# Kernel tuning notes

Measured on AMD Instinct MI355X. Metric: run time of the kernel, lower is better.

The kernel has to match this reference:

```python
import jax, jax.numpy as jnp
import numpy as np

B, T, I, H = 64, 2048, 256, 256  # batch, timesteps, input_dim, units


def setup_inputs() -> dict:
    key = jax.random.key(0)
    k1, k2, k3 = jax.random.split(key, 3)
    scale_x = 1.0 / np.sqrt(I)
    scale_h = 1.0 / np.sqrt(H)
    return {
        "x": jax.random.normal(k1, (B, T, I), dtype=jnp.float32),
        "Wx": jax.random.normal(k2, (I, 4 * H), dtype=jnp.float32) * scale_x,
        "Wh": jax.random.normal(k3, (H, 4 * H), dtype=jnp.float32) * scale_h,
        "b": jnp.zeros((4 * H,), dtype=jnp.float32),
        "h0": jnp.zeros((B, H), dtype=jnp.float32),
        "c0": jnp.zeros((B, H), dtype=jnp.float32),
    }


def reference(x, Wx, Wh, b, h0, c0):
    """Keras RNN(LSTMCell, return_sequences=True): sequential scan over time.

    Gate order follows Keras LSTM: i, f, c(g), o with sigmoid recurrent
    activation and tanh cell activation.
    """
    H_ = h0.shape[-1]
    # Input projection is time-independent: hoist out of the scan. [B,T,4H]
    xz = jnp.einsum("bti,ig->btg", x, Wx) + b

    def step(carry, xz_t):
        h, c = carry
        z = xz_t + h @ Wh  # [B,4H]
        i = jax.nn.sigmoid(z[:, 0 * H_:1 * H_])
        f = jax.nn.sigmoid(z[:, 1 * H_:2 * H_])
        g = jnp.tanh(z[:, 2 * H_:3 * H_])
        o = jax.nn.sigmoid(z[:, 3 * H_:4 * H_])
        c_new = f * c + i * g
        h_new = o * jnp.tanh(c_new)
        return (h_new, c_new), h_new

    # scan over time axis: [T,B,4H]
    (_, _), outputs = jax.lax.scan(step, (h0, c0), jnp.transpose(xz, (1, 0, 2)))
    return jnp.transpose(outputs, (1, 0, 2))  # [B,T,H]
```

## Files before the change

### kernel.cpp

```cpp
#include <hip/hip_runtime.h>

typedef unsigned short u16;
typedef unsigned int   u32;
typedef short short8 __attribute__((ext_vector_type(8)));
typedef float f32x4  __attribute__((ext_vector_type(4)));
typedef u32   u32x4  __attribute__((ext_vector_type(4)));

#define AGENT __HIP_MEMORY_SCOPE_AGENT

__device__ __forceinline__ float bf2f(u16 u) {
    u32 x = ((u32)u) << 16;
    return __builtin_bit_cast(float, x);
}
__device__ __forceinline__ u16 f2bf(float f) {
    u32 x = __builtin_bit_cast(u32, f);
    u32 r = (x + 0x7FFFu + ((x >> 16) & 1u)) >> 16;
    return (u16)r;
}
__device__ __forceinline__ float sigmoidf_(float x) { return 1.0f / (1.0f + __expf(-x)); }
__device__ __forceinline__ float tanhf_(float x) { return 2.0f / (1.0f + __expf(-2.0f * x)) - 1.0f; }

__device__ __forceinline__ int xcd_load_i32(const int* p) {
    int v;
    asm volatile("global_load_dword %0, %1, off sc0\n\t"
                 "s_waitcnt vmcnt(0)"
                 : "=v"(v) : "v"(p) : "memory");
    return v;
}
__device__ __forceinline__ void xcd_atomic_add(int* p, int v) {
    asm volatile("global_atomic_add %0, %1, off" :: "v"(p), "v"(v) : "memory");
}
__device__ __forceinline__ void xcd_load_32B(const void* p, u32* hv) {
    u32x4 a, b;
    asm volatile("global_load_dwordx4 %0, %2, off sc0\n\t"
                 "global_load_dwordx4 %1, %2, off offset:16 sc0\n\t"
                 "s_waitcnt vmcnt(0)"
                 : "=&v"(a), "=&v"(b) : "v"(p) : "memory");
    hv[0] = a.x; hv[1] = a.y; hv[2] = a.z; hv[3] = a.w;
    hv[4] = b.x; hv[5] = b.y; hv[6] = b.z; hv[7] = b.w;
}

__global__ __launch_bounds__(256) void lstm_init(const u16* __restrict__ xbits,
                                                 int* __restrict__ ints) {
    int t = threadIdx.x;
    ints[t] = 0;
    ints[t + 256] = 0;
    if (t == 0) {
        int cnt = 0;
        const uint4* p = (const uint4*)xbits;
        for (int j = 0; j < 64; j++) {
            uint4 v = p[j];
            u32 wv[4] = {v.x, v.y, v.z, v.w};
#pragma unroll
            for (int k2 = 0; k2 < 4; k2++) {
                u32 lo = wv[k2] & 0xFFFFu, hi = wv[k2] >> 16;
                cnt += ((lo & 0x7F80u) >= 0x4600u) ? 1 : 0;
                cnt += ((hi & 0x7F80u) >= 0x4600u) ? 1 : 0;
            }
        }
        ints[0] = cnt;
    }
}

__global__ __launch_bounds__(256, 1) void lstm_fused(const void* __restrict__ x,
                                                     const void* __restrict__ Wx,
                                                     const void* __restrict__ Wh,
                                                     const void* __restrict__ bias,
                                                     const void* __restrict__ c0,
                                                     const void* __restrict__ h0,
                                                     u16* __restrict__ hbuf,
                                                     void* __restrict__ out,
                                                     int* __restrict__ ints) {
    __shared__ __align__(16) u16 hs[16 * 264];
    __shared__ int sb[3];

    const int tid = threadIdx.x;
    const int lane = tid & 63, w = tid >> 6;
    const int q = lane >> 4, n16 = lane & 15;

    if (tid == 0) {
        int* xslots  = ints + 8;
        int* claimed = ints + 16;
        int* mxcd    = ints + 32;
        int* okv     = ints + 48;
        int xcd = __builtin_amdgcn_s_getreg((3u << 11) | 20) & 7;
        int g = -1, mm = -1;
        int slot = __hip_atomic_fetch_add(&xslots[xcd], 1, __ATOMIC_RELAXED, AGENT);
        if (xcd < 4 && slot < 4) {
            int id = xcd * 4 + slot;
            __hip_atomic_store(&mxcd[id], xcd, __ATOMIC_RELEASE, AGENT);
            int exp0 = 0;
            if (__hip_atomic_compare_exchange_strong(&claimed[id], &exp0, 1,
                    __ATOMIC_ACQ_REL, __ATOMIC_RELAXED, AGENT)) { g = xcd; mm = slot; }
        } else {
            int seq = __hip_atomic_fetch_add(&ints[1], 1, __ATOMIC_RELAXED, AGENT);
            if (seq < 16) {
                int seen = 0;
                for (int it = 0; it < 4096; ++it) {
                    if (__hip_atomic_load(&claimed[seq], __ATOMIC_RELAXED, AGENT)) { seen = 1; break; }
                    __builtin_amdgcn_s_sleep(32);
                }
                if (!seen) {
                    __hip_atomic_store(&mxcd[seq], 64, __ATOMIC_RELEASE, AGENT);
                    int exp0 = 0;
                    if (__hip_atomic_compare_exchange_strong(&claimed[seq], &exp0, 2,
                            __ATOMIC_ACQ_REL, __ATOMIC_RELAXED, AGENT)) { g = seq >> 2; mm = seq & 3; }
                }
            }
        }
        int fast = 0;
        if (g >= 0) {
            if (mm == 0) {
                int all = 1;
                for (int k = 1; k < 4; ++k) {
                    int it = 0;
                    while (!__hip_atomic_load(&claimed[g * 4 + k], __ATOMIC_ACQUIRE, AGENT)) {
                        __builtin_amdgcn_s_sleep(16);
                        if (++it > (1 << 19)) { all = 0; break; }
                    }
                }
                int myx = __hip_atomic_load(&mxcd[g * 4 + 0], __ATOMIC_RELAXED, AGENT);
                if (all) {
                    fast = 1;
                    for (int k = 1; k < 4; ++k)
                        if (__hip_atomic_load(&mxcd[g * 4 + k], __ATOMIC_RELAXED, AGENT) != myx) fast = 0;
                }
                __hip_atomic_store(&okv[g], fast ? 1 : 2, __ATOMIC_RELEASE, AGENT);
            }
            int it = 0, o;
            while ((o = __hip_atomic_load(&okv[g], __ATOMIC_ACQUIRE, AGENT)) == 0) {
                __builtin_amdgcn_s_sleep(16);
                if (++it > (1 << 20)) { o = 2; break; }
            }
            fast = (o == 1);
        }
        sb[0] = g; sb[1] = mm; sb[2] = fast;
    }
    __syncthreads();
    const int jB = sb[0], jH = sb[1], fast = sb[2];
    if (jB < 0) return;

    const int b0 = jB * 16;
    const int hc = jH * 64 + w * 16 + n16;
    const int bq = b0 + q * 4;

    const int isf32 = (ints[0] > 64);
    int* const ctrp = ints + 64 + jB * 64;
    u16* const hgrp = hbuf + (size_t)jB * 8192;

    short8 Bh[4][8];
    short8 Bx[4][8];

#define PRELOAD_W(Wsrc, Bf)                                                    \
    _Pragma("unroll")                                                          \
    for (int p = 0; p < 16; p++) {                                             \
        const int g = p >> 2, sub = p & 3;                                     \
        const int colg = g * 256 + jH * 64 + sub * 16;                         \
        u16 tmp[16];                                                           \
        if (isf32) {                                                           \
            const float* s = (const float*)(Wsrc) + (size_t)tid * 1024 + colg; \
            _Pragma("unroll")                                                  \
            for (int c = 0; c < 16; c++) tmp[c] = f2bf(s[c]);                  \
        } else {                                                               \
            const u16* s = (const u16*)(Wsrc) + (size_t)tid * 1024 + colg;     \
            *(uint4*)&tmp[0] = *(const uint4*)s;                               \
            *(uint4*)&tmp[8] = *(const uint4*)(s + 8);                         \
        }                                                                      \
        __syncthreads();                        \
        _Pragma("unroll")                                                      \
        for (int c = 0; c < 16; c++) hs[c * 264 + tid] = tmp[c];               \
        __syncthreads();                                                       \
        if (sub == w) {                                                        \
            _Pragma("unroll")                                                  \
            for (int ks = 0; ks < 8; ks++)                                     \
                (Bf)[g][ks] = *(const short8*)&hs[n16 * 264 + ks * 32 + q * 8];\
        }                                                                      \
    }

    PRELOAD_W(Wh, Bh)
    PRELOAD_W(Wx, Bx)
    __syncthreads();

#define LOADX(t, dst)                                                              \
    if (isf32) {                                                                   \
        const float* xb = (const float*)x + ((size_t)(b0 + n16) * 2048 + (t)) * 256 + q * 8; \
        _Pragma("unroll")                                                          \
        for (int ks = 0; ks < 8; ks++) {                                           \
            u16 tmp[8];                                                            \
            _Pragma("unroll")                                                      \
            for (int j = 0; j < 8; j++) tmp[j] = f2bf(xb[ks * 32 + j]);            \
            (dst)[ks] = *(const short8*)tmp;                                       \
        }                                                                          \
    } else {                                                                       \
        const u16* xb = (const u16*)x + ((size_t)(b0 + n16) * 2048 + (t)) * 256 + q * 8; \
        _Pragma("unroll")                                                          \
        for (int ks = 0; ks < 8; ks++) (dst)[ks] = *(const short8*)(xb + ks * 32); \
    }

    float bv[4];
#pragma unroll
    for (int g = 0; g < 4; g++)
        bv[g] = isf32 ? ((const float*)bias)[g * 256 + hc]
                      : bf2f(((const u16*)bias)[g * 256 + hc]);

    float creg[4];
#pragma unroll
    for (int r = 0; r < 4; r++)
        creg[r] = isf32 ? ((const float*)c0)[(size_t)(bq + r) * 256 + hc]
                        : bf2f(((const u16*)c0)[(size_t)(bq + r) * 256 + hc]);

#pragma unroll
    for (int m = 0; m < 16; m++) {
        u16 v = isf32 ? f2bf(((const float*)h0)[(size_t)(b0 + m) * 256 + tid])
                      : ((const u16*)h0)[(size_t)(b0 + m) * 256 + tid];
        hs[m * 264 + tid] = v;
    }

    f32x4 zx[4];
    {
        short8 xf[8];
        LOADX(0, xf)
#pragma unroll
        for (int g = 0; g < 4; g++) { f32x4 a = {bv[g], bv[g], bv[g], bv[g]}; zx[g] = a; }
#pragma unroll
        for (int ks = 0; ks < 8; ks++)
#pragma unroll
            for (int g = 0; g < 4; g++)
                zx[g] = __builtin_amdgcn_mfma_f32_16x16x32_bf16(xf[ks], Bx[g][ks], zx[g], 0, 0, 0);
    }

    int dead = 0;

    for (int tl = 0; tl < 2048; tl++) {
        short8 xfn[8];
        if (tl + 1 < 2048) { LOADX(tl + 1, xfn) }

        if (tl > 0) {
            const int target = 4 * tl;
            if (!dead) {
                int guard = 0;
                if (fast) {
                    while (xcd_load_i32(ctrp) < target) {
                        __builtin_amdgcn_s_sleep(1);
                        if (++guard > (1 << 20)) { dead = 1; break; }
                    }
                } else {
                    while (__hip_atomic_load(ctrp, __ATOMIC_ACQUIRE, AGENT) < target) {
                        __builtin_amdgcn_s_sleep(1);
                        if (++guard > (1 << 20)) { dead = 1; break; }
                    }
                }
            }
            const int par = (tl & 1) ^ 1;
            const u16* hp = hgrp + par * 4096 + tid * 16;
            u32 hv[8];
            if (fast) {
                xcd_load_32B(hp, hv);
            } else {
                const u32* hp32 = (const u32*)hp;
#pragma unroll
                for (int i2 = 0; i2 < 8; i2++) hv[i2] = __hip_atomic_load(hp32 + i2, __ATOMIC_RELAXED, AGENT);
            }
#pragma unroll
            for (int m = 0; m < 16; m++) {
                u16 val = (u16)((hv[m >> 1] >> ((m & 1) * 16)) & 0xFFFFu);
                hs[m * 264 + tid] = val;
            }
        }
        __syncthreads();

        f32x4 acc[4];
#pragma unroll
        for (int g = 0; g < 4; g++) acc[g] = zx[g];
#pragma unroll
        for (int ks = 0; ks < 8; ks++) {
            short8 af = *(const short8*)&hs[n16 * 264 + ks * 32 + q * 8];
#pragma unroll
            for (int g = 0; g < 4; g++)
                acc[g] = __builtin_amdgcn_mfma_f32_16x16x32_bf16(af, Bh[g][ks], acc[g], 0, 0, 0);
        }

        float hf[4];
        u16 hb[4];
#pragma unroll
        for (int r = 0; r < 4; r++) {
            float ig = sigmoidf_(acc[0][r]);
            float fg = sigmoidf_(acc[1][r]);
            float gg = tanhf_(acc[2][r]);
            float og = sigmoidf_(acc[3][r]);
            float cn = fg * creg[r] + ig * gg;
            creg[r] = cn;
            hf[r] = og * tanhf_(cn);
            hb[r] = f2bf(hf[r]);
        }
        {
            const int par = tl & 1;
            u32* hp = (u32*)(hgrp + par * 4096 + hc * 16 + q * 4);
            u32 lo = (u32)hb[0] | ((u32)hb[1] << 16);
            u32 hi = (u32)hb[2] | ((u32)hb[3] << 16);
            if (fast) {
                hp[0] = lo;
                hp[1] = hi;
            } else {
                __hip_atomic_store(hp + 0, lo, __ATOMIC_RELAXED, AGENT);
                __hip_atomic_store(hp + 1, hi, __ATOMIC_RELAXED, AGENT);
            }
        }
        __syncthreads();
        if (tid == 0) {
            if (fast) xcd_atomic_add(ctrp, 1);
            else __hip_atomic_fetch_add(ctrp, 1, __ATOMIC_RELEASE, AGENT);
        }

#pragma unroll
        for (int r = 0; r < 4; r++) {
            size_t oi = ((size_t)(bq + r) * 2048 + tl) * 256 + hc;
            if (isf32) ((float*)out)[oi] = hf[r];
            else       ((u16*)out)[oi] = hb[r];
        }

        if (tl + 1 < 2048) {
#pragma unroll
            for (int g = 0; g < 4; g++) { f32x4 a = {bv[g], bv[g], bv[g], bv[g]}; zx[g] = a; }
#pragma unroll
            for (int ks = 0; ks < 8; ks++)
#pragma unroll
                for (int g = 0; g < 4; g++)
                    zx[g] = __builtin_amdgcn_mfma_f32_16x16x32_bf16(xfn[ks], Bx[g][ks], zx[g], 0, 0, 0);
        }
    }
}

extern "C" void kernel_launch(void* const* d_in, const int* in_sizes, int n_in,
                              void* d_out, int out_size, void* d_ws, size_t ws_size,
                              hipStream_t stream) {
    const void* x    = d_in[0];
    const void* Wx   = d_in[1];
    const void* Wh   = d_in[2];
    const void* bias = d_in[3];
    const void* h0   = d_in[4];
    const void* c0   = d_in[5];

    u16* hbuf = (u16*)d_ws;
    int* ints = (int*)((char*)d_ws + 65536);

    lstm_init<<<1, 256, 0, stream>>>((const u16*)x, ints);
    lstm_fused<<<256, 256, 0, stream>>>(x, Wx, Wh, bias, c0, h0, hbuf, d_out, ints);
}
```

Before: 13.40 ms.

## Replace cross-block hidden-state exchange with single 1024-thread block per batch group

The kernel previously split each 16-row batch group across four 256-thread blocks that traded hidden state through global memory, using atomic counters and spin-waits with XCD-placement detection. Now each batch group runs in one 1024-thread workgroup, so the hidden state is exchanged through double-buffered LDS with a single barrier per timestep. The input projection is computed in-loop from LDS-staged x, with the next step's x prefetched into registers. This removes the global round-trips and atomics from the recurrence critical path. In exchange it launches only 4 blocks and adds the x-projection MFMAs to the serial per-step chain.

```diff
diff --git a/kernel.cpp b/kernel.cpp
--- a/kernel.cpp
+++ b/kernel.cpp
@@ -4,9 +4,6 @@
 typedef unsigned int   u32;
 typedef short short8 __attribute__((ext_vector_type(8)));
 typedef float f32x4  __attribute__((ext_vector_type(4)));
-typedef u32   u32x4  __attribute__((ext_vector_type(4)));
-
-#define AGENT __HIP_MEMORY_SCOPE_AGENT
 
 __device__ __forceinline__ float bf2f(u16 u) {
     u32 x = ((u32)u) << 16;
@@ -20,32 +17,9 @@
 __device__ __forceinline__ float sigmoidf_(float x) { return 1.0f / (1.0f + __expf(-x)); }
 __device__ __forceinline__ float tanhf_(float x) { return 2.0f / (1.0f + __expf(-2.0f * x)) - 1.0f; }
 
-__device__ __forceinline__ int xcd_load_i32(const int* p) {
-    int v;
-    asm volatile("global_load_dword %0, %1, off sc0\n\t"
-                 "s_waitcnt vmcnt(0)"
-                 : "=v"(v) : "v"(p) : "memory");
-    return v;
-}
-__device__ __forceinline__ void xcd_atomic_add(int* p, int v) {
-    asm volatile("global_atomic_add %0, %1, off" :: "v"(p), "v"(v) : "memory");
-}
-__device__ __forceinline__ void xcd_load_32B(const void* p, u32* hv) {
-    u32x4 a, b;
-    asm volatile("global_load_dwordx4 %0, %2, off sc0\n\t"
-                 "global_load_dwordx4 %1, %2, off offset:16 sc0\n\t"
-                 "s_waitcnt vmcnt(0)"
-                 : "=&v"(a), "=&v"(b) : "v"(p) : "memory");
-    hv[0] = a.x; hv[1] = a.y; hv[2] = a.z; hv[3] = a.w;
-    hv[4] = b.x; hv[5] = b.y; hv[6] = b.z; hv[7] = b.w;
-}
-
-__global__ __launch_bounds__(256) void lstm_init(const u16* __restrict__ xbits,
-                                                 int* __restrict__ ints) {
-    int t = threadIdx.x;
-    ints[t] = 0;
-    ints[t + 256] = 0;
-    if (t == 0) {
+__global__ __launch_bounds__(64) void lstm_init(const u16* __restrict__ xbits,
+                                                int* __restrict__ flag) {
+    if (threadIdx.x == 0) {
         int cnt = 0;
         const uint4* p = (const uint4*)xbits;
         for (int j = 0; j < 64; j++) {
@@ -58,143 +32,64 @@
                 cnt += ((hi & 0x7F80u) >= 0x4600u) ? 1 : 0;
             }
         }
-        ints[0] = cnt;
-    }
-}
-
-__global__ __launch_bounds__(256, 1) void lstm_fused(const void* __restrict__ x,
-                                                     const void* __restrict__ Wx,
-                                                     const void* __restrict__ Wh,
-                                                     const void* __restrict__ bias,
-                                                     const void* __restrict__ c0,
-                                                     const void* __restrict__ h0,
-                                                     u16* __restrict__ hbuf,
-                                                     void* __restrict__ out,
-                                                     int* __restrict__ ints) {
-    __shared__ __align__(16) u16 hs[16 * 264];
-    __shared__ int sb[3];
+        *flag = cnt;
+    }
+}
+
+__global__ __launch_bounds__(1024) void lstm_fused(const void* __restrict__ x,
+                                                   const void* __restrict__ Wx,
+                                                   const void* __restrict__ Wh,
+                                                   const void* __restrict__ bias,
+                                                   const void* __restrict__ c0,
+                                                   const void* __restrict__ h0,
+                                                   void* __restrict__ out,
+                                                   const int* __restrict__ flag) {
+    __shared__ __align__(16) u16 hsb2[2][16 * 264];
+    __shared__ __align__(16) u16 xsb2[2][16 * 264];
 
     const int tid = threadIdx.x;
     const int lane = tid & 63, w = tid >> 6;
     const int q = lane >> 4, n16 = lane & 15;
-
-    if (tid == 0) {
-        int* xslots  = ints + 8;
-        int* claimed = ints + 16;
-        int* mxcd    = ints + 32;
-        int* okv     = ints + 48;
-        int xcd = __builtin_amdgcn_s_getreg((3u << 11) | 20) & 7;
-        int g = -1, mm = -1;
-        int slot = __hip_atomic_fetch_add(&xslots[xcd], 1, __ATOMIC_RELAXED, AGENT);
-        if (xcd < 4 && slot < 4) {
-            int id = xcd * 4 + slot;
-            __hip_atomic_store(&mxcd[id], xcd, __ATOMIC_RELEASE, AGENT);
-            int exp0 = 0;
-            if (__hip_atomic_compare_exchange_strong(&claimed[id], &exp0, 1,
-                    __ATOMIC_ACQ_REL, __ATOMIC_RELAXED, AGENT)) { g = xcd; mm = slot; }
-        } else {
-            int seq = __hip_atomic_fetch_add(&ints[1], 1, __ATOMIC_RELAXED, AGENT);
-            if (seq < 16) {
-                int seen = 0;
-                for (int it = 0; it < 4096; ++it) {
-                    if (__hip_atomic_load(&claimed[seq], __ATOMIC_RELAXED, AGENT)) { seen = 1; break; }
-                    __builtin_amdgcn_s_sleep(32);
+    const int b0 = blockIdx.x * 16;
+    const int hc = w * 16 + n16;
+    const int bq = b0 + q * 4;
+    const int ms = tid >> 6;
+    const int k0 = (tid & 63) * 4;
+
+    const int isf32 = (*flag > 64);
+
+    const float* xf32 = (const float*)x;
+    const u16*   xb16 = (const u16*)x;
+
+    short8 Bh[4][8];
+    short8 Bx[4][8];
+#pragma unroll
+    for (int g = 0; g < 4; g++) {
+#pragma unroll
+        for (int ks = 0; ks < 8; ks++) {
+            const int col = g * 256 + hc;
+            const int kr = ks * 32 + q * 8;
+            u16 th[8], tx[8];
+            if (isf32) {
+                const float* whf = (const float*)Wh;
+                const float* wxf = (const float*)Wx;
+#pragma unroll
+                for (int j = 0; j < 8; j++) {
+                    th[j] = f2bf(whf[(size_t)(kr + j) * 1024 + col]);
+                    tx[j] = f2bf(wxf[(size_t)(kr + j) * 1024 + col]);
                 }
-                if (!seen) {
-                    __hip_atomic_store(&mxcd[seq], 64, __ATOMIC_RELEASE, AGENT);
-                    int exp0 = 0;
-                    if (__hip_atomic_compare_exchange_strong(&claimed[seq], &exp0, 2,
-                            __ATOMIC_ACQ_REL, __ATOMIC_RELAXED, AGENT)) { g = seq >> 2; mm = seq & 3; }
+            } else {
+                const u16* whu = (const u16*)Wh;
+                const u16* wxu = (const u16*)Wx;
+#pragma unroll
+                for (int j = 0; j < 8; j++) {
+                    th[j] = whu[(size_t)(kr + j) * 1024 + col];
+                    tx[j] = wxu[(size_t)(kr + j) * 1024 + col];
                 }
             }
-        }
-        int fast = 0;
-        if (g >= 0) {
-            if (mm == 0) {
-                int all = 1;
-                for (int k = 1; k < 4; ++k) {
-                    int it = 0;
-                    while (!__hip_atomic_load(&claimed[g * 4 + k], __ATOMIC_ACQUIRE, AGENT)) {
-                        __builtin_amdgcn_s_sleep(16);
-                        if (++it > (1 << 19)) { all = 0; break; }
-                    }
-                }
-                int myx = __hip_atomic_load(&mxcd[g * 4 + 0], __ATOMIC_RELAXED, AGENT);
-                if (all) {
-                    fast = 1;
-                    for (int k = 1; k < 4; ++k)
-                        if (__hip_atomic_load(&mxcd[g * 4 + k], __ATOMIC_RELAXED, AGENT) != myx) fast = 0;
-                }
-                __hip_atomic_store(&okv[g], fast ? 1 : 2, __ATOMIC_RELEASE, AGENT);
-            }
-            int it = 0, o;
-            while ((o = __hip_atomic_load(&okv[g], __ATOMIC_ACQUIRE, AGENT)) == 0) {
-                __builtin_amdgcn_s_sleep(16);
-                if (++it > (1 << 20)) { o = 2; break; }
-            }
-            fast = (o == 1);
-        }
-        sb[0] = g; sb[1] = mm; sb[2] = fast;
-    }
-    __syncthreads();
-    const int jB = sb[0], jH = sb[1], fast = sb[2];
-    if (jB < 0) return;
-
-    const int b0 = jB * 16;
-    const int hc = jH * 64 + w * 16 + n16;
-    const int bq = b0 + q * 4;
-
-    const int isf32 = (ints[0] > 64);
-    int* const ctrp = ints + 64 + jB * 64;
-    u16* const hgrp = hbuf + (size_t)jB * 8192;
-
-    short8 Bh[4][8];
-    short8 Bx[4][8];
-
-#define PRELOAD_W(Wsrc, Bf)                                                    \
-    _Pragma("unroll")                                                          \
-    for (int p = 0; p < 16; p++) {                                             \
-        const int g = p >> 2, sub = p & 3;                                     \
-        const int colg = g * 256 + jH * 64 + sub * 16;                         \
-        u16 tmp[16];                                                           \
-        if (isf32) {                                                           \
-            const float* s = (const float*)(Wsrc) + (size_t)tid * 1024 + colg; \
-            _Pragma("unroll")                                                  \
-            for (int c = 0; c < 16; c++) tmp[c] = f2bf(s[c]);                  \
-        } else {                                                               \
-            const u16* s = (const u16*)(Wsrc) + (size_t)tid * 1024 + colg;     \
-            *(uint4*)&tmp[0] = *(const uint4*)s;                               \
-            *(uint4*)&tmp[8] = *(const uint4*)(s + 8);                         \
-        }                                                                      \
-        __syncthreads();                        \
-        _Pragma("unroll")                                                      \
-        for (int c = 0; c < 16; c++) hs[c * 264 + tid] = tmp[c];               \
-        __syncthreads();                                                       \
-        if (sub == w) {                                                        \
-            _Pragma("unroll")                                                  \
-            for (int ks = 0; ks < 8; ks++)                                     \
-                (Bf)[g][ks] = *(const short8*)&hs[n16 * 264 + ks * 32 + q * 8];\
-        }                                                                      \
-    }
-
-    PRELOAD_W(Wh, Bh)
-    PRELOAD_W(Wx, Bx)
-    __syncthreads();
-
-#define LOADX(t, dst)                                                              \
-    if (isf32) {                                                                   \
-        const float* xb = (const float*)x + ((size_t)(b0 + n16) * 2048 + (t)) * 256 + q * 8; \
-        _Pragma("unroll")                                                          \
-        for (int ks = 0; ks < 8; ks++) {                                           \
-            u16 tmp[8];                                                            \
-            _Pragma("unroll")                                                      \
-            for (int j = 0; j < 8; j++) tmp[j] = f2bf(xb[ks * 32 + j]);            \
-            (dst)[ks] = *(const short8*)tmp;                                       \
-        }                                                                          \
-    } else {                                                                       \
-        const u16* xb = (const u16*)x + ((size_t)(b0 + n16) * 2048 + (t)) * 256 + q * 8; \
-        _Pragma("unroll")                                                          \
-        for (int ks = 0; ks < 8; ks++) (dst)[ks] = *(const short8*)(xb + ks * 32); \
+            Bh[g][ks] = *(const short8*)th;
+            Bx[g][ks] = *(const short8*)tx;
+        }
     }
 
     float bv[4];
@@ -209,79 +104,77 @@
         creg[r] = isf32 ? ((const float*)c0)[(size_t)(bq + r) * 256 + hc]
                         : bf2f(((const u16*)c0)[(size_t)(bq + r) * 256 + hc]);
 
-#pragma unroll
-    for (int m = 0; m < 16; m++) {
-        u16 v = isf32 ? f2bf(((const float*)h0)[(size_t)(b0 + m) * 256 + tid])
-                      : ((const u16*)h0)[(size_t)(b0 + m) * 256 + tid];
-        hs[m * 264 + tid] = v;
-    }
-
-    f32x4 zx[4];
     {
-        short8 xf[8];
-        LOADX(0, xf)
-#pragma unroll
-        for (int g = 0; g < 4; g++) { f32x4 a = {bv[g], bv[g], bv[g], bv[g]}; zx[g] = a; }
-#pragma unroll
-        for (int ks = 0; ks < 8; ks++)
+        u16 hv[4], xv[4];
+        if (isf32) {
+            const float* hp = (const float*)h0 + (size_t)(b0 + ms) * 256 + k0;
+            const float* xp = xf32 + ((size_t)(b0 + ms) * 2048 + 0) * 256 + k0;
+#pragma unroll
+            for (int j = 0; j < 4; j++) { hv[j] = f2bf(hp[j]); xv[j] = f2bf(xp[j]); }
+        } else {
+            const u16* hp = (const u16*)h0 + (size_t)(b0 + ms) * 256 + k0;
+            const u16* xp = xb16 + ((size_t)(b0 + ms) * 2048 + 0) * 256 + k0;
+#pragma unroll
+            for (int j = 0; j < 4; j++) { hv[j] = hp[j]; xv[j] = xp[j]; }
+        }
+        u32 hlo = (u32)hv[0] | ((u32)hv[1] << 16), hhi = (u32)hv[2] | ((u32)hv[3] << 16);
+        u32 xlo = (u32)xv[0] | ((u32)xv[1] << 16), xhi = (u32)xv[2] | ((u32)xv[3] << 16);
+        *(uint2*)&hsb2[0][ms * 264 + k0] = make_uint2(hlo, hhi);
+        *(uint2*)&xsb2[0][ms * 264 + k0] = make_uint2(xlo, xhi);
+    }
+    __syncthreads();
+
+    float4 xpf = make_float4(0.f, 0.f, 0.f, 0.f);
+    uint2  xpb = make_uint2(0, 0);
+
+    float hf[4];
+    u16 hb[4] = {0, 0, 0, 0};
+
+    for (int tl = 0; tl < 2048; tl++) {
+        u16* hsb = hsb2[tl & 1];
+        u16* xsb = xsb2[tl & 1];
+
+        if (tl > 0) {
+#pragma unroll
+            for (int r = 0; r < 4; r++) hsb[(q * 4 + r) * 264 + hc] = hb[r];
+            u16 xv[4];
+            if (isf32) {
+                xv[0] = f2bf(xpf.x); xv[1] = f2bf(xpf.y);
+                xv[2] = f2bf(xpf.z); xv[3] = f2bf(xpf.w);
+            } else {
+                xv[0] = (u16)(xpb.x & 0xFFFFu); xv[1] = (u16)(xpb.x >> 16);
+                xv[2] = (u16)(xpb.y & 0xFFFFu); xv[3] = (u16)(xpb.y >> 16);
+            }
+            u32 xlo = (u32)xv[0] | ((u32)xv[1] << 16), xhi = (u32)xv[2] | ((u32)xv[3] << 16);
+            *(uint2*)&xsb[ms * 264 + k0] = make_uint2(xlo, xhi);
+        }
+        if (tl + 1 < 2048) {
+            if (isf32)
+                xpf = *(const float4*)&xf32[((size_t)(b0 + ms) * 2048 + (tl + 1)) * 256 + k0];
+            else
+                xpb = *(const uint2*)&xb16[((size_t)(b0 + ms) * 2048 + (tl + 1)) * 256 + k0];
+        }
+
+        asm volatile("s_waitcnt lgkmcnt(0)\n\ts_barrier" ::: "memory");
+
+        f32x4 acc[4];
+#pragma unroll
+        for (int g = 0; g < 4; g++) { f32x4 a = {bv[g], bv[g], bv[g], bv[g]}; acc[g] = a; }
+#pragma unroll
+        for (int ks = 0; ks < 8; ks++) {
+            short8 af = *(const short8*)&xsb[n16 * 264 + ks * 32 + q * 8];
 #pragma unroll
             for (int g = 0; g < 4; g++)
-                zx[g] = __builtin_amdgcn_mfma_f32_16x16x32_bf16(xf[ks], Bx[g][ks], zx[g], 0, 0, 0);
-    }
-
-    int dead = 0;
-
-    for (int tl = 0; tl < 2048; tl++) {
-        short8 xfn[8];
-        if (tl + 1 < 2048) { LOADX(tl + 1, xfn) }
-
-        if (tl > 0) {
-            const int target = 4 * tl;
-            if (!dead) {
-                int guard = 0;
-                if (fast) {
-                    while (xcd_load_i32(ctrp) < target) {
-                        __builtin_amdgcn_s_sleep(1);
-                        if (++guard > (1 << 20)) { dead = 1; break; }
-                    }
-                } else {
-                    while (__hip_atomic_load(ctrp, __ATOMIC_ACQUIRE, AGENT) < target) {
-                        __builtin_amdgcn_s_sleep(1);
-                        if (++guard > (1 << 20)) { dead = 1; break; }
-                    }
-                }
-            }
-            const int par = (tl & 1) ^ 1;
-            const u16* hp = hgrp + par * 4096 + tid * 16;
-            u32 hv[8];
-            if (fast) {
-                xcd_load_32B(hp, hv);
-            } else {
-                const u32* hp32 = (const u32*)hp;
-#pragma unroll
-                for (int i2 = 0; i2 < 8; i2++) hv[i2] = __hip_atomic_load(hp32 + i2, __ATOMIC_RELAXED, AGENT);
-            }
-#pragma unroll
-            for (int m = 0; m < 16; m++) {
-                u16 val = (u16)((hv[m >> 1] >> ((m & 1) * 16)) & 0xFFFFu);
-                hs[m * 264 + tid] = val;
-            }
-        }
-        __syncthreads();
-
-        f32x4 acc[4];
-#pragma unroll
-        for (int g = 0; g < 4; g++) acc[g] = zx[g];
+                acc[g] = __builtin_amdgcn_mfma_f32_16x16x32_bf16(af, Bx[g][ks], acc[g], 0, 0, 0);
+        }
 #pragma unroll
         for (int ks = 0; ks < 8; ks++) {
-            short8 af = *(const short8*)&hs[n16 * 264 + ks * 32 + q * 8];
+            short8 af = *(const short8*)&hsb[n16 * 264 + ks * 32 + q * 8];
 #pragma unroll
             for (int g = 0; g < 4; g++)
                 acc[g] = __builtin_amdgcn_mfma_f32_16x16x32_bf16(af, Bh[g][ks], acc[g], 0, 0, 0);
         }
 
-        float hf[4];
-        u16 hb[4];
 #pragma unroll
         for (int r = 0; r < 4; r++) {
             float ig = sigmoidf_(acc[0][r]);
@@ -293,40 +186,12 @@
             hf[r] = og * tanhf_(cn);
             hb[r] = f2bf(hf[r]);
         }
-        {
-            const int par = tl & 1;
-            u32* hp = (u32*)(hgrp + par * 4096 + hc * 16 + q * 4);
-            u32 lo = (u32)hb[0] | ((u32)hb[1] << 16);
-            u32 hi = (u32)hb[2] | ((u32)hb[3] << 16);
-            if (fast) {
-                hp[0] = lo;
-                hp[1] = hi;
-            } else {
-                __hip_atomic_store(hp + 0, lo, __ATOMIC_RELAXED, AGENT);
-                __hip_atomic_store(hp + 1, hi, __ATOMIC_RELAXED, AGENT);
-            }
-        }
-        __syncthreads();
-        if (tid == 0) {
-            if (fast) xcd_atomic_add(ctrp, 1);
-            else __hip_atomic_fetch_add(ctrp, 1, __ATOMIC_RELEASE, AGENT);
-        }
 
 #pragma unroll
         for (int r = 0; r < 4; r++) {
             size_t oi = ((size_t)(bq + r) * 2048 + tl) * 256 + hc;
             if (isf32) ((float*)out)[oi] = hf[r];
             else       ((u16*)out)[oi] = hb[r];
-        }
-
-        if (tl + 1 < 2048) {
-#pragma unroll
-            for (int g = 0; g < 4; g++) { f32x4 a = {bv[g], bv[g], bv[g], bv[g]}; zx[g] = a; }
-#pragma unroll
-            for (int ks = 0; ks < 8; ks++)
-#pragma unroll
-                for (int g = 0; g < 4; g++)
-                    zx[g] = __builtin_amdgcn_mfma_f32_16x16x32_bf16(xfn[ks], Bx[g][ks], zx[g], 0, 0, 0);
         }
     }
 }
@@ -341,9 +206,8 @@
     const void* h0   = d_in[4];
     const void* c0   = d_in[5];
 
-    u16* hbuf = (u16*)d_ws;
-    int* ints = (int*)((char*)d_ws + 65536);
-
-    lstm_init<<<1, 256, 0, stream>>>((const u16*)x, ints);
-    lstm_fused<<<256, 256, 0, stream>>>(x, Wx, Wh, bias, c0, h0, hbuf, d_out, ints);
-}
+    int* flag = (int*)d_ws;
+
+    lstm_init<<<1, 64, 0, stream>>>((const u16*)x, flag);
+    lstm_fused<<<4, 1024, 0, stream>>>(x, Wx, Wh, bias, c0, h0, d_out, flag);
+}
```

New measurement: 48.04 ms. 258% more time.
